# Kernel tuning notes

Measured on AMD Instinct MI355X. Metric: run time of the kernel, lower is better.

Reference implementation:

```python
import jax, jax.numpy as jnp
import numpy as np

KERNEL = 3
PAD = KERNEL // 2


def setup_inputs() -> dict:
    key = jax.random.key(0)
    k1, k2, k3, k4 = jax.random.split(key, 4)
    B, Cin, Cout, D = 2, 32, 64, 64
    x = jax.random.normal(k1, (B, Cin, D, D, D), dtype=jnp.float32)
    mask = jax.random.randint(k2, (B, D, D, D), 0, 2).astype(jnp.bool_)
    fan_in = Cin * KERNEL ** 3
    bound = 1.0 / np.sqrt(fan_in)
    weight = jax.random.uniform(k3, (Cout, Cin, KERNEL, KERNEL, KERNEL),
                                dtype=jnp.float32, minval=-bound, maxval=bound)
    bias = jax.random.uniform(k4, (Cout,), dtype=jnp.float32, minval=-bound, maxval=bound)
    return {"x": x, "mask": mask, "weight": weight, "bias": bias}


def reference(x, mask, weight, bias):
    # Dense conv3d with 'same' padding, then zero out unoccupied voxels
    # (the CUDA warp kernel only computes occupied voxels; others are 0).
    out = jax.lax.conv_general_dilated(
        x, weight,
        window_strides=(1, 1, 1),
        padding=[(PAD, PAD)] * 3,
        dimension_numbers=("NCDHW", "OIDHW", "NCDHW"),
    )
    out = out + bias[None, :, None, None, None]
    return out * mask[:, None, :, :, :].astype(out.dtype)
```

## Files before the change

### kernel.cpp

```cpp
#include <hip/hip_runtime.h>
#include <stdint.h>


#define DD 64
#define CIN 32
#define COUT 64

typedef __bf16 bf16x8 __attribute__((ext_vector_type(8)));
typedef float f32x16 __attribute__((ext_vector_type(16)));

#define XT_BYTES (2u * 64u * 64u * 64u * 32u * 2u)
#define WPK_U16  (27 * 2 * 2 * 64 * 8)
#define WS_NEEDED (XT_BYTES + (size_t)WPK_U16 * 2)
#define CONV_LDS  (18 * 4224)

__device__ __forceinline__ uint16_t f2bf(float f) {
    uint32_t u = __builtin_bit_cast(uint32_t, f);
    u += 0x7fffu + ((u >> 16) & 1u);
    return (uint16_t)(u >> 16);
}

__global__ void pack_weights(const float* __restrict__ w, uint16_t* __restrict__ wpk) {
    int flat = blockIdx.x * 256 + threadIdx.x;
    if (flat >= WPK_U16) return;
    int j   = flat & 7;
    int l   = (flat >> 3) & 63;
    int ct  = (flat >> 9) & 1;
    int cb  = (flat >> 10) & 1;
    int k27 = flat >> 11;
    int co = ct * 32 + (l & 31);
    int ci = cb * 16 + ((l >> 5) * 8) + j;
    wpk[flat] = f2bf(w[(co * CIN + ci) * 27 + k27]);
}

__global__ __launch_bounds__(256)
void transpose_x(const float* __restrict__ x, uint16_t* __restrict__ xt) {
    __shared__ uint16_t tile[2048];
    const int y = blockIdx.x, z = blockIdx.y, b = blockIdx.z;
    const int t = threadIdx.x;
    const int ci = t >> 3;
    const int xs = (t & 7) * 8;
    const float* src = x + ((((size_t)b * CIN + ci) * DD + z) * DD + y) * DD + xs;
    float4 v0 = *(const float4*)src;
    float4 v1 = *(const float4*)(src + 4);
    float vals[8] = {v0.x, v0.y, v0.z, v0.w, v1.x, v1.y, v1.z, v1.w};
#pragma unroll
    for (int e = 0; e < 8; ++e) {
        int xv = xs + e;
        int pos = xv * 32 + (((ci >> 3) ^ ((xv >> 1) & 3)) << 3) + (ci & 7);
        tile[pos] = f2bf(vals[e]);
    }
    __syncthreads();
    uint16_t* dst = xt + (((size_t)b * DD + z) * DD + y) * 2048;
    ((uint4*)dst)[t] = ((const uint4*)tile)[t];
}

__global__ __launch_bounds__(512, 4)
void conv_mfma(const uint16_t* __restrict__ xt, const uint16_t* __restrict__ wpk,
               const int* __restrict__ mask, const float* __restrict__ bias,
               float* __restrict__ out) {
    extern __shared__ __align__(16) unsigned char lds[];
    const int yq = blockIdx.x, z = blockIdx.y, b = blockIdx.z;
    const int y0 = yq * 4;
    const int tid = threadIdx.x;
    const int lane = tid & 63;
    const int w = __builtin_amdgcn_readfirstlane(tid >> 6);
    const int ct = w & 1;
    const int xtile = (w >> 1) & 1;
    const int wy = w >> 2;

    for (int i = tid; i < 144; i += 512) {
        int row = i >> 3, side = (i >> 2) & 1, k = i & 3;
        *(uint4*)&lds[row * 4224 + side * 4160 + k * 16] = make_uint4(0, 0, 0, 0);
    }
    for (int i = w; i < 72; i += 8) {
        int row = i >> 2, kc = i & 3;
        int zz = z - 1 + (row / 6);
        int yy = y0 - 1 + (row % 6);
        uint4 v = make_uint4(0, 0, 0, 0);
        if (zz >= 0 && zz < DD && yy >= 0 && yy < DD)
            v = *(const uint4*)(xt + (((size_t)b * DD + zz) * DD + yy) * 2048 + kc * 512 + lane * 8);
        *(uint4*)&lds[row * 4224u + 64u + kc * 1024u + lane * 16u] = v;
    }
    __syncthreads();

    const int u = lane & 31;
    const int h = lane >> 5;
    const int ya = y0 + 2 * wy;
    const int xoff = xtile * 32;

    f32x16 accA, accB;
#pragma unroll
    for (int i = 0; i < 16; ++i) { accA[i] = 0.f; accB[i] = 0.f; }

#pragma unroll
    for (int zr = 0; zr < 3; ++zr) {
#pragma unroll
        for (int cb = 0; cb < 2; ++cb) {
            bf16x8 wf[9];
#pragma unroll
            for (int q = 0; q < 9; ++q) {
                const int k27 = zr * 9 + q;
                wf[q] = *(const bf16x8*)(wpk + (size_t)((k27 * 2 + cb) * 2 + ct) * 512 + lane * 8);
            }
            const unsigned cc = (unsigned)(cb * 2 + h);
#pragma unroll
            for (int t = 0; t < 4; ++t) {
                const unsigned rb = (unsigned)((zr * 6 + 2 * wy + t) * 4224);
                bf16x8 bf[3];
#pragma unroll
                for (int kx = 0; kx < 3; ++kx) {
                    const unsigned sl = (unsigned)(xoff + u + kx);
                    const unsigned s = ((sl - 1u) >> 1) & 3u;
                    bf[kx] = *(const bf16x8*)&lds[rb + sl * 64u + ((cc ^ s) << 4)];
                }
                if (t <= 2) {
#pragma unroll
                    for (int kx = 0; kx < 3; ++kx)
                        accA = __builtin_amdgcn_mfma_f32_32x32x16_bf16(wf[t * 3 + kx], bf[kx], accA, 0, 0, 0);
                }
                if (t >= 1) {
#pragma unroll
                    for (int kx = 0; kx < 3; ++kx)
                        accB = __builtin_amdgcn_mfma_f32_32x32x16_bf16(wf[(t - 1) * 3 + kx], bf[kx], accB, 0, 0, 0);
                }
            }
        }
    }

    const size_t mb0 = (((size_t)b * DD + z) * DD + ya) * DD;
    const float m0 = mask[mb0 + xoff + u]      ? 1.0f : 0.0f;
    const float m1 = mask[mb0 + DD + xoff + u] ? 1.0f : 0.0f;
#pragma unroll
    for (int r = 0; r < 16; ++r) {
        const int co = ct * 32 + (r & 3) + 8 * (r >> 2) + 4 * h;
        const float bs = bias[co];
        const size_t o = ((size_t)b * COUT + co) * (DD * DD * DD)
                       + (size_t)z * (DD * DD) + (size_t)ya * DD + xoff;
        out[o + u]      = (accA[r] + bs) * m0;
        out[o + DD + u] = (accB[r] + bs) * m1;
    }
}

#define CI_BLK 16
__global__ __launch_bounds__(256, 2)
void sparse_conv3d_f32(const float* __restrict__ x,
                       const int* __restrict__ mask,
                       const float* __restrict__ weight,
                       const float* __restrict__ bias,
                       float* __restrict__ out) {
    __shared__ float lds[9 * CI_BLK * 66];
    const int y = blockIdx.x, z = blockIdx.y, b = blockIdx.z;
    const int lane = threadIdx.x & 63;
    const int wave = __builtin_amdgcn_readfirstlane(threadIdx.x >> 6);
    float acc[16];
#pragma unroll
    for (int j = 0; j < 16; ++j) acc[j] = 0.0f;
    const int co0 = wave * 16;
    const float* wbase = weight + (size_t)co0 * (CIN * 27);
    for (int cbl = 0; cbl < 2; ++cbl) {
        if (cbl) __syncthreads();
        for (int i = wave; i < 9 * CI_BLK; i += 4) {
            const int r = i >> 4, ci_l = i & 15;
            const int zz = z + (r / 3) - 1, yy = y + (r % 3) - 1;
            const int ci = cbl * CI_BLK + ci_l;
            float v = 0.0f;
            if (zz >= 0 && zz < DD && yy >= 0 && yy < DD)
                v = x[((((size_t)b * CIN + ci) * DD + zz) * DD + yy) * DD + lane];
            float* row = &lds[(size_t)i * 66];
            row[1 + lane] = v;
            if (lane == 0) { row[0] = 0.0f; row[65] = 0.0f; }
        }
        __syncthreads();
        for (int ci_l = 0; ci_l < CI_BLK; ++ci_l) {
            const int ci = cbl * CI_BLK + ci_l;
#pragma unroll
            for (int kz = 0; kz < 3; ++kz) {
#pragma unroll
                for (int ky = 0; ky < 3; ++ky) {
                    const int r = kz * 3 + ky;
                    const float* xrow = &lds[(size_t)(r * CI_BLK + ci_l) * 66 + lane];
                    const float xv0 = xrow[0], xv1 = xrow[1], xv2 = xrow[2];
                    const float* wp = wbase + ci * 27 + kz * 9 + ky * 3;
#pragma unroll
                    for (int j = 0; j < 16; ++j) {
                        acc[j] += wp[(size_t)j * (CIN * 27) + 0] * xv0
                                + wp[(size_t)j * (CIN * 27) + 1] * xv1
                                + wp[(size_t)j * (CIN * 27) + 2] * xv2;
                    }
                }
            }
        }
    }
    const float m = mask[(((size_t)b * DD + z) * DD + y) * DD + lane] ? 1.0f : 0.0f;
#pragma unroll
    for (int j = 0; j < 16; ++j) {
        const int co = co0 + j;
        out[((((size_t)b * COUT + co) * DD + z) * DD + y) * DD + lane] = (acc[j] + bias[co]) * m;
    }
}

extern "C" void kernel_launch(void* const* d_in, const int* in_sizes, int n_in,
                              void* d_out, int out_size, void* d_ws, size_t ws_size,
                              hipStream_t stream) {
    const float* x    = (const float*)d_in[0];
    const int*   mask = (const int*)d_in[1];
    const float* w    = (const float*)d_in[2];
    const float* bias = (const float*)d_in[3];
    float*       out  = (float*)d_out;

    if (ws_size < WS_NEEDED) {
        sparse_conv3d_f32<<<dim3(DD, DD, 2), 256, 0, stream>>>(x, mask, w, bias, out);
        return;
    }

    uint16_t* xt  = (uint16_t*)d_ws;
    uint16_t* wpk = (uint16_t*)((char*)d_ws + XT_BYTES);

    pack_weights<<<(WPK_U16 + 255) / 256, 256, 0, stream>>>(w, wpk);
    transpose_x<<<dim3(DD, DD, 2), 256, 0, stream>>>(x, xt);
    conv_mfma<<<dim3(DD / 4, DD, 2), 512, CONV_LDS, stream>>>(xt, wpk, mask, bias, out);
}
```

Measured before the change: 92.93 us.

## Double-buffer z-slices via direct global-to-LDS loads with 4-row accumulators per wave

The conv kernel now runs 4 waves per block instead of 8, and each wave accumulates all 4 output rows so every loaded input row feeds more MFMAs. The input halo is staged one z-slice at a time into two LDS buffers using global_load_lds. Loading the next slice overlaps with compute on the current one. Out-of-range rows read from a zeroed page instead of taking a branch. The trade-offs are more accumulator registers per wave, lower occupancy bounds, and less parallelism per block.

Result: faster. 88.79 us (-4.5%).

```diff
diff --git a/kernel.cpp b/kernel.cpp
--- a/kernel.cpp
+++ b/kernel.cpp
@@ -9,10 +9,13 @@
 typedef __bf16 bf16x8 __attribute__((ext_vector_type(8)));
 typedef float f32x16 __attribute__((ext_vector_type(16)));
 
-#define XT_BYTES (2u * 64u * 64u * 64u * 32u * 2u)
-#define WPK_U16  (27 * 2 * 2 * 64 * 8)
-#define WS_NEEDED (XT_BYTES + (size_t)WPK_U16 * 2)
-#define CONV_LDS  (18 * 4224)
+#define XT_BYTES  (2u * 64u * 64u * 64u * 32u * 2u)
+#define WPK_U16   (27 * 2 * 2 * 64 * 8)
+#define WPK_BYTES ((size_t)WPK_U16 * 2)
+#define ZP_BYTES  1024
+#define WS_NEEDED (XT_BYTES + WPK_BYTES + ZP_BYTES)
+#define BUF_STRIDE 25344u
+#define CONV_LDS  (2 * 25344)
 
 __device__ __forceinline__ uint16_t f2bf(float f) {
     uint32_t u = __builtin_bit_cast(uint32_t, f);
@@ -20,17 +23,27 @@
     return (uint16_t)(u >> 16);
 }
 
-__global__ void pack_weights(const float* __restrict__ w, uint16_t* __restrict__ wpk) {
+__device__ __forceinline__ void gll16(const void* g, void* l) {
+    __builtin_amdgcn_global_load_lds(
+        (__attribute__((address_space(1))) void*)g,
+        (__attribute__((address_space(3))) void*)l, 16, 0, 0);
+}
+
+__global__ void pack_weights(const float* __restrict__ w, uint16_t* __restrict__ wpk,
+                             uint4* __restrict__ zp) {
     int flat = blockIdx.x * 256 + threadIdx.x;
-    if (flat >= WPK_U16) return;
-    int j   = flat & 7;
-    int l   = (flat >> 3) & 63;
-    int ct  = (flat >> 9) & 1;
-    int cb  = (flat >> 10) & 1;
-    int k27 = flat >> 11;
-    int co = ct * 32 + (l & 31);
-    int ci = cb * 16 + ((l >> 5) * 8) + j;
-    wpk[flat] = f2bf(w[(co * CIN + ci) * 27 + k27]);
+    if (flat < WPK_U16) {
+        int j   = flat & 7;
+        int l   = (flat >> 3) & 63;
+        int ct  = (flat >> 9) & 1;
+        int cb  = (flat >> 10) & 1;
+        int k27 = flat >> 11;
+        int co = ct * 32 + (l & 31);
+        int ci = cb * 16 + ((l >> 5) * 8) + j;
+        wpk[flat] = f2bf(w[(co * CIN + ci) * 27 + k27]);
+    } else if (flat - WPK_U16 < ZP_BYTES / 16) {
+        zp[flat - WPK_U16] = make_uint4(0, 0, 0, 0);
+    }
 }
 
 __global__ __launch_bounds__(256)
@@ -55,8 +68,9 @@
     ((uint4*)dst)[t] = ((const uint4*)tile)[t];
 }
 
-__global__ __launch_bounds__(512, 4)
+__global__ __launch_bounds__(256, 3)
 void conv_mfma(const uint16_t* __restrict__ xt, const uint16_t* __restrict__ wpk,
+               const uint16_t* __restrict__ zp,
                const int* __restrict__ mask, const float* __restrict__ bias,
                float* __restrict__ out) {
     extern __shared__ __align__(16) unsigned char lds[];
@@ -65,80 +79,88 @@
     const int tid = threadIdx.x;
     const int lane = tid & 63;
     const int w = __builtin_amdgcn_readfirstlane(tid >> 6);
-    const int ct = w & 1;
+    const int ct    = w & 1;
     const int xtile = (w >> 1) & 1;
-    const int wy = w >> 2;
-
-    for (int i = tid; i < 144; i += 512) {
-        int row = i >> 3, side = (i >> 2) & 1, k = i & 3;
-        *(uint4*)&lds[row * 4224 + side * 4160 + k * 16] = make_uint4(0, 0, 0, 0);
-    }
-    for (int i = w; i < 72; i += 8) {
-        int row = i >> 2, kc = i & 3;
-        int zz = z - 1 + (row / 6);
-        int yy = y0 - 1 + (row % 6);
-        uint4 v = make_uint4(0, 0, 0, 0);
-        if (zz >= 0 && zz < DD && yy >= 0 && yy < DD)
-            v = *(const uint4*)(xt + (((size_t)b * DD + zz) * DD + yy) * 2048 + kc * 512 + lane * 8);
-        *(uint4*)&lds[row * 4224u + 64u + kc * 1024u + lane * 16u] = v;
-    }
-    __syncthreads();
-
     const int u = lane & 31;
     const int h = lane >> 5;
-    const int ya = y0 + 2 * wy;
     const int xoff = xtile * 32;
 
-    f32x16 accA, accB;
-#pragma unroll
-    for (int i = 0; i < 16; ++i) { accA[i] = 0.f; accB[i] = 0.f; }
-
-#pragma unroll
-    for (int zr = 0; zr < 3; ++zr) {
-#pragma unroll
-        for (int cb = 0; cb < 2; ++cb) {
-            bf16x8 wf[9];
-#pragma unroll
-            for (int q = 0; q < 9; ++q) {
-                const int k27 = zr * 9 + q;
-                wf[q] = *(const bf16x8*)(wpk + (size_t)((k27 * 2 + cb) * 2 + ct) * 512 + lane * 8);
-            }
-            const unsigned cc = (unsigned)(cb * 2 + h);
-#pragma unroll
-            for (int t = 0; t < 4; ++t) {
-                const unsigned rb = (unsigned)((zr * 6 + 2 * wy + t) * 4224);
-                bf16x8 bf[3];
-#pragma unroll
-                for (int kx = 0; kx < 3; ++kx) {
-                    const unsigned sl = (unsigned)(xoff + u + kx);
-                    const unsigned s = ((sl - 1u) >> 1) & 3u;
-                    bf[kx] = *(const bf16x8*)&lds[rb + sl * 64u + ((cc ^ s) << 4)];
-                }
-                if (t <= 2) {
-#pragma unroll
-                    for (int kx = 0; kx < 3; ++kx)
-                        accA = __builtin_amdgcn_mfma_f32_32x32x16_bf16(wf[t * 3 + kx], bf[kx], accA, 0, 0, 0);
-                }
-                if (t >= 1) {
-#pragma unroll
-                    for (int kx = 0; kx < 3; ++kx)
-                        accB = __builtin_amdgcn_mfma_f32_32x32x16_bf16(wf[(t - 1) * 3 + kx], bf[kx], accB, 0, 0, 0);
-                }
-            }
-        }
-    }
-
-    const size_t mb0 = (((size_t)b * DD + z) * DD + ya) * DD;
-    const float m0 = mask[mb0 + xoff + u]      ? 1.0f : 0.0f;
-    const float m1 = mask[mb0 + DD + xoff + u] ? 1.0f : 0.0f;
+    if (tid < 96) {
+        int bb = tid >= 48, j = tid - bb * 48;
+        int row = j >> 3, side = (j >> 2) & 1, k = j & 3;
+        *(uint4*)&lds[bb * BUF_STRIDE + row * 4224 + side * 4160 + k * 16] = make_uint4(0, 0, 0, 0);
+    }
+
+#define STAGE(zrp, bufbase)                                                          \
+    {   const int zz_ = z - 1 + (zrp);                                               \
+        _Pragma("unroll") for (int c_ = 0; c_ < 6; ++c_) {                           \
+            const int chunk_ = c_ * 4 + w;                                           \
+            const int row_ = chunk_ >> 2, kc_ = chunk_ & 3;                          \
+            const int yy_ = y0 - 1 + row_;                                           \
+            const uint16_t* src_ = (zz_ >= 0 && zz_ < DD && yy_ >= 0 && yy_ < DD)    \
+                ? xt + (((size_t)b * DD + zz_) * DD + yy_) * 2048 + kc_ * 512 + lane * 8 \
+                : zp + lane * 8;                                                     \
+            gll16(src_, &lds[(bufbase) + row_ * 4224u + 64u + kc_ * 1024u]);         \
+        }                                                                            \
+    }
+
+    f32x16 acc[4];
+#pragma unroll
+    for (int ly = 0; ly < 4; ++ly)
+#pragma unroll
+        for (int i = 0; i < 16; ++i) acc[ly][i] = 0.f;
+
+#define PHASE(zr, bufbase)                                                           \
+    _Pragma("unroll") for (int cb_ = 0; cb_ < 2; ++cb_) {                            \
+        bf16x8 wf[9];                                                                \
+        _Pragma("unroll") for (int q_ = 0; q_ < 9; ++q_)                             \
+            wf[q_] = *(const bf16x8*)(wpk + (size_t)((((zr) * 9 + q_) * 2 + cb_) * 2 + ct) * 512 + lane * 8); \
+        const unsigned cc_ = (unsigned)(cb_ * 2 + h);                                \
+        _Pragma("unroll") for (int t_ = 0; t_ < 6; ++t_) {                           \
+            const unsigned rb_ = (unsigned)((bufbase) + t_ * 4224u);                 \
+            bf16x8 bf[3];                                                            \
+            _Pragma("unroll") for (int kx_ = 0; kx_ < 3; ++kx_) {                    \
+                const unsigned sl_ = (unsigned)(xoff + u + kx_);                     \
+                const unsigned s_ = ((sl_ - 1u) >> 1) & 3u;                          \
+                bf[kx_] = *(const bf16x8*)&lds[rb_ + sl_ * 64u + ((cc_ ^ s_) << 4)]; \
+            }                                                                        \
+            _Pragma("unroll") for (int ly_ = 0; ly_ < 4; ++ly_) {                    \
+                const int ky_ = t_ - ly_;                                            \
+                if (ky_ >= 0 && ky_ <= 2) {                                          \
+                    _Pragma("unroll") for (int kx_ = 0; kx_ < 3; ++kx_)              \
+                        acc[ly_] = __builtin_amdgcn_mfma_f32_32x32x16_bf16(          \
+                            wf[ky_ * 3 + kx_], bf[kx_], acc[ly_], 0, 0, 0);          \
+                }                                                                    \
+            }                                                                        \
+        }                                                                            \
+    }
+
+    STAGE(0, 0u)
+    STAGE(1, BUF_STRIDE)
+    __syncthreads();
+    PHASE(0, 0u)
+    __syncthreads();
+    STAGE(2, 0u)
+    PHASE(1, BUF_STRIDE)
+    __syncthreads();
+    PHASE(2, 0u)
+
+#undef STAGE
+#undef PHASE
+
+    const size_t mb0 = (((size_t)b * DD + z) * DD + y0) * DD + xoff + u;
+    float m[4];
+#pragma unroll
+    for (int ly = 0; ly < 4; ++ly) m[ly] = mask[mb0 + ly * DD] ? 1.0f : 0.0f;
 #pragma unroll
     for (int r = 0; r < 16; ++r) {
         const int co = ct * 32 + (r & 3) + 8 * (r >> 2) + 4 * h;
         const float bs = bias[co];
         const size_t o = ((size_t)b * COUT + co) * (DD * DD * DD)
-                       + (size_t)z * (DD * DD) + (size_t)ya * DD + xoff;
-        out[o + u]      = (accA[r] + bs) * m0;
-        out[o + DD + u] = (accB[r] + bs) * m1;
+                       + (size_t)z * (DD * DD) + (size_t)y0 * DD + xoff + u;
+#pragma unroll
+        for (int ly = 0; ly < 4; ++ly)
+            out[o + ly * DD] = (acc[ly][r] + bs) * m[ly];
     }
 }
 
@@ -216,8 +238,9 @@
 
     uint16_t* xt  = (uint16_t*)d_ws;
     uint16_t* wpk = (uint16_t*)((char*)d_ws + XT_BYTES);
-
-    pack_weights<<<(WPK_U16 + 255) / 256, 256, 0, stream>>>(w, wpk);
+    uint16_t* zp  = (uint16_t*)((char*)d_ws + XT_BYTES + WPK_BYTES);
+
+    pack_weights<<<(WPK_U16 + ZP_BYTES / 16 + 255) / 256, 256, 0, stream>>>(w, wpk, (uint4*)zp);
     transpose_x<<<dim3(DD, DD, 2), 256, 0, stream>>>(x, xt);
-    conv_mfma<<<dim3(DD / 4, DD, 2), 512, CONV_LDS, stream>>>(xt, wpk, mask, bias, out);
-}
+    conv_mfma<<<dim3(DD / 4, DD, 2), 256, CONV_LDS, stream>>>(xt, wpk, zp, mask, bias, out);
+}
```

## Drop LDS staging; read padded bf16 input directly and compute 4 rows x 64 channels per wave

Applied to the files above, without the earlier changes.

The transpose kernel now writes a y- and x-padded channels-last bf16 layout with zeroed halo rows, so the conv kernel can skip bounds checks. The conv kernel no longer stages input in LDS. Each wave reads B fragments straight from global/L2 and accumulates 4 output rows for both output-channel tiles, so every loaded fragment feeds up to 8 MFMAs. This removes LDS fill and the barrier and raises register-level reuse. The cost is 8 accumulator tiles in registers, lower occupancy, unswizzled strided global loads, and a larger padded workspace.

Result: slower. 140.2 us (+50.9%).

```diff
diff --git a/kernel.cpp b/kernel.cpp
--- a/kernel.cpp
+++ b/kernel.cpp
@@ -9,10 +9,11 @@
 typedef __bf16 bf16x8 __attribute__((ext_vector_type(8)));
 typedef float f32x16 __attribute__((ext_vector_type(16)));
 
-#define XT_BYTES (2u * 64u * 64u * 64u * 32u * 2u)
-#define WPK_U16  (27 * 2 * 2 * 64 * 8)
+#define ROW_U16   2112u
+#define XT_U16    ((size_t)2 * 64 * 66 * ROW_U16)
+#define XT_BYTES  (XT_U16 * 2)
+#define WPK_U16   (27 * 2 * 2 * 64 * 8)
 #define WS_NEEDED (XT_BYTES + (size_t)WPK_U16 * 2)
-#define CONV_LDS  (18 * 4224)
 
 __device__ __forceinline__ uint16_t f2bf(float f) {
     uint32_t u = __builtin_bit_cast(uint32_t, f);
@@ -35,9 +36,16 @@
 
 __global__ __launch_bounds__(256)
 void transpose_x(const float* __restrict__ x, uint16_t* __restrict__ xt) {
-    __shared__ uint16_t tile[2048];
-    const int y = blockIdx.x, z = blockIdx.y, b = blockIdx.z;
+    __shared__ uint16_t tile[ROW_U16];
+    const int yy = blockIdx.x, z = blockIdx.y, b = blockIdx.z;
+    const int y = yy - 1;
     const int t = threadIdx.x;
+    uint4* dst = (uint4*)(xt + ((size_t)(b * DD + z) * 66 + yy) * ROW_U16);
+
+    if (y < 0 || y >= DD) {
+        for (int i = t; i < 264; i += 256) dst[i] = make_uint4(0, 0, 0, 0);
+        return;
+    }
     const int ci = t >> 3;
     const int xs = (t & 7) * 8;
     const float* src = x + ((((size_t)b * CIN + ci) * DD + z) * DD + y) * DD + xs;
@@ -45,100 +53,89 @@
     float4 v1 = *(const float4*)(src + 4);
     float vals[8] = {v0.x, v0.y, v0.z, v0.w, v1.x, v1.y, v1.z, v1.w};
 #pragma unroll
-    for (int e = 0; e < 8; ++e) {
-        int xv = xs + e;
-        int pos = xv * 32 + (((ci >> 3) ^ ((xv >> 1) & 3)) << 3) + (ci & 7);
-        tile[pos] = f2bf(vals[e]);
-    }
+    for (int e = 0; e < 8; ++e)
+        tile[(xs + e + 1) * 32 + ci] = f2bf(vals[e]);
+    if (t < 32) { tile[t] = 0; tile[65 * 32 + t] = 0; }
     __syncthreads();
-    uint16_t* dst = xt + (((size_t)b * DD + z) * DD + y) * 2048;
-    ((uint4*)dst)[t] = ((const uint4*)tile)[t];
-}
-
-__global__ __launch_bounds__(512, 4)
+    for (int i = t; i < 264; i += 256) dst[i] = ((const uint4*)tile)[i];
+}
+
+__global__ __launch_bounds__(256, 2)
 void conv_mfma(const uint16_t* __restrict__ xt, const uint16_t* __restrict__ wpk,
                const int* __restrict__ mask, const float* __restrict__ bias,
                float* __restrict__ out) {
-    extern __shared__ __align__(16) unsigned char lds[];
-    const int yq = blockIdx.x, z = blockIdx.y, b = blockIdx.z;
-    const int y0 = yq * 4;
+    const int yo = blockIdx.x, z = blockIdx.y, b = blockIdx.z;
     const int tid = threadIdx.x;
     const int lane = tid & 63;
     const int w = __builtin_amdgcn_readfirstlane(tid >> 6);
-    const int ct = w & 1;
-    const int xtile = (w >> 1) & 1;
-    const int wy = w >> 2;
-
-    for (int i = tid; i < 144; i += 512) {
-        int row = i >> 3, side = (i >> 2) & 1, k = i & 3;
-        *(uint4*)&lds[row * 4224 + side * 4160 + k * 16] = make_uint4(0, 0, 0, 0);
-    }
-    for (int i = w; i < 72; i += 8) {
-        int row = i >> 2, kc = i & 3;
-        int zz = z - 1 + (row / 6);
-        int yy = y0 - 1 + (row % 6);
-        uint4 v = make_uint4(0, 0, 0, 0);
-        if (zz >= 0 && zz < DD && yy >= 0 && yy < DD)
-            v = *(const uint4*)(xt + (((size_t)b * DD + zz) * DD + yy) * 2048 + kc * 512 + lane * 8);
-        *(uint4*)&lds[row * 4224u + 64u + kc * 1024u + lane * 16u] = v;
-    }
-    __syncthreads();
-
+    const int xtile = w & 1;
+    const int y0 = (yo * 2 + (w >> 1)) * 4;
     const int u = lane & 31;
     const int h = lane >> 5;
-    const int ya = y0 + 2 * wy;
     const int xoff = xtile * 32;
 
-    f32x16 accA, accB;
-#pragma unroll
-    for (int i = 0; i < 16; ++i) { accA[i] = 0.f; accB[i] = 0.f; }
-
-#pragma unroll
-    for (int zr = 0; zr < 3; ++zr) {
+    f32x16 acc[4][2];
+#pragma unroll
+    for (int ly = 0; ly < 4; ++ly)
+#pragma unroll
+        for (int ct = 0; ct < 2; ++ct)
+#pragma unroll
+            for (int i = 0; i < 16; ++i) acc[ly][ct][i] = 0.f;
+
+    for (int p = 0; p < 3; ++p) {
+        const int zz = z - 1 + p;
+        if (zz < 0 || zz >= DD) continue;
+        const uint16_t* plane = xt + (size_t)(b * DD + zz) * 66 * ROW_U16;
 #pragma unroll
         for (int cb = 0; cb < 2; ++cb) {
-            bf16x8 wf[9];
+            bf16x8 wf[9][2];
 #pragma unroll
             for (int q = 0; q < 9; ++q) {
-                const int k27 = zr * 9 + q;
-                wf[q] = *(const bf16x8*)(wpk + (size_t)((k27 * 2 + cb) * 2 + ct) * 512 + lane * 8);
+                const int k27 = p * 9 + q;
+                wf[q][0] = *(const bf16x8*)(wpk + (size_t)((k27 * 2 + cb) * 2 + 0) * 512 + lane * 8);
+                wf[q][1] = *(const bf16x8*)(wpk + (size_t)((k27 * 2 + cb) * 2 + 1) * 512 + lane * 8);
             }
-            const unsigned cc = (unsigned)(cb * 2 + h);
-#pragma unroll
-            for (int t = 0; t < 4; ++t) {
-                const unsigned rb = (unsigned)((zr * 6 + 2 * wy + t) * 4224);
+            const unsigned chunk = (unsigned)((cb * 2 + h) * 8);
+#pragma unroll
+            for (int t = 0; t < 6; ++t) {
+                const uint16_t* rowp = plane + (size_t)(y0 + t) * ROW_U16 + chunk;
                 bf16x8 bf[3];
 #pragma unroll
+                for (int kx = 0; kx < 3; ++kx)
+                    bf[kx] = *(const bf16x8*)(rowp + (unsigned)(xoff + u + kx) * 32);
+#pragma unroll
                 for (int kx = 0; kx < 3; ++kx) {
-                    const unsigned sl = (unsigned)(xoff + u + kx);
-                    const unsigned s = ((sl - 1u) >> 1) & 3u;
-                    bf[kx] = *(const bf16x8*)&lds[rb + sl * 64u + ((cc ^ s) << 4)];
-                }
-                if (t <= 2) {
-#pragma unroll
-                    for (int kx = 0; kx < 3; ++kx)
-                        accA = __builtin_amdgcn_mfma_f32_32x32x16_bf16(wf[t * 3 + kx], bf[kx], accA, 0, 0, 0);
-                }
-                if (t >= 1) {
-#pragma unroll
-                    for (int kx = 0; kx < 3; ++kx)
-                        accB = __builtin_amdgcn_mfma_f32_32x32x16_bf16(wf[(t - 1) * 3 + kx], bf[kx], accB, 0, 0, 0);
+#pragma unroll
+                    for (int ly = 0; ly < 4; ++ly) {
+                        const int ky = t - ly;
+                        if (ky >= 0 && ky < 3) {
+                            acc[ly][0] = __builtin_amdgcn_mfma_f32_32x32x16_bf16(
+                                wf[ky * 3 + kx][0], bf[kx], acc[ly][0], 0, 0, 0);
+                            acc[ly][1] = __builtin_amdgcn_mfma_f32_32x32x16_bf16(
+                                wf[ky * 3 + kx][1], bf[kx], acc[ly][1], 0, 0, 0);
+                        }
+                    }
                 }
             }
         }
     }
 
-    const size_t mb0 = (((size_t)b * DD + z) * DD + ya) * DD;
-    const float m0 = mask[mb0 + xoff + u]      ? 1.0f : 0.0f;
-    const float m1 = mask[mb0 + DD + xoff + u] ? 1.0f : 0.0f;
+    const size_t mb = (((size_t)b * DD + z) * DD + y0) * DD + xoff + u;
+    float m[4];
+#pragma unroll
+    for (int ly = 0; ly < 4; ++ly) m[ly] = mask[mb + ly * DD] ? 1.0f : 0.0f;
 #pragma unroll
     for (int r = 0; r < 16; ++r) {
-        const int co = ct * 32 + (r & 3) + 8 * (r >> 2) + 4 * h;
-        const float bs = bias[co];
-        const size_t o = ((size_t)b * COUT + co) * (DD * DD * DD)
-                       + (size_t)z * (DD * DD) + (size_t)ya * DD + xoff;
-        out[o + u]      = (accA[r] + bs) * m0;
-        out[o + DD + u] = (accB[r] + bs) * m1;
+#pragma unroll
+        for (int ct = 0; ct < 2; ++ct) {
+            const int co = ct * 32 + (r & 3) + 8 * (r >> 2) + 4 * h;
+            const float bs = bias[co];
+            const size_t o = ((size_t)b * COUT + co) * (DD * DD * DD)
+                           + (size_t)z * (DD * DD) + (size_t)y0 * DD + xoff + u;
+#pragma unroll
+            for (int ly = 0; ly < 4; ++ly)
+                out[o + ly * DD] = (acc[ly][ct][r] + bs) * m[ly];
+        }
     }
 }
 
@@ -199,6 +196,7 @@
         out[((((size_t)b * COUT + co) * DD + z) * DD + y) * DD + lane] = (acc[j] + bias[co]) * m;
     }
 }
+#undef CI_BLK
 
 extern "C" void kernel_launch(void* const* d_in, const int* in_sizes, int n_in,
                               void* d_out, int out_size, void* d_ws, size_t ws_size,
@@ -218,6 +216,6 @@
     uint16_t* wpk = (uint16_t*)((char*)d_ws + XT_BYTES);
 
     pack_weights<<<(WPK_U16 + 255) / 256, 256, 0, stream>>>(w, wpk);
-    transpose_x<<<dim3(DD, DD, 2), 256, 0, stream>>>(x, xt);
-    conv_mfma<<<dim3(DD / 4, DD, 2), 512, CONV_LDS, stream>>>(xt, wpk, mask, bias, out);
-}
+    transpose_x<<<dim3(66, DD, 2), 256, 0, stream>>>(x, xt);
+    conv_mfma<<<dim3(DD / 8, DD, 2), 256, 0, stream>>>(xt, wpk, mask, bias, out);
+}
```
